# Optimization experiments

Measured on AMD Instinct MI355X. Metric: run time of the kernel, lower is better.

Reference implementation:

```python
import jax, jax.numpy as jnp
import numpy as np

B, N, C = 4, 2048, 320
H, D = 5, 64            # heads, dim_head
INNER = H * D           # 320


def setup_inputs() -> dict:
    key = jax.random.key(0)
    ks = jax.random.split(key, 7)
    x = jax.random.normal(ks[0], (B, N, C), dtype=jnp.float32)
    edge = jax.random.uniform(ks[1], (B, N, 1), dtype=jnp.float32)
    s = 1.0 / np.sqrt(C)
    Wq = jax.random.normal(ks[2], (C, INNER), dtype=jnp.float32) * s
    Wk = jax.random.normal(ks[3], (C, INNER), dtype=jnp.float32) * s
    Wv = jax.random.normal(ks[4], (C, INNER), dtype=jnp.float32) * s
    Wo = jax.random.normal(ks[5], (INNER, C), dtype=jnp.float32) * (1.0 / np.sqrt(INNER))
    bo = jnp.zeros((C,), dtype=jnp.float32)
    return {"x": x, "edge": edge, "Wq": Wq, "Wk": Wk, "Wv": Wv, "Wo": Wo, "bo": bo}


def _split_heads(t):
    # 'b n (h d) -> (b h) n d'  (batch-major, head-minor)
    b, n, _ = t.shape
    return t.reshape(b, n, H, D).transpose(0, 2, 1, 3).reshape(b * H, n, D)


def reference(x, edge, Wq, Wk, Wv, Wo, bo):
    scale = D ** -0.5
    q = _split_heads(x @ Wq).astype(jnp.float32)   # (B*H, N, D)
    k = _split_heads(x @ Wk).astype(jnp.float32)
    v = _split_heads(x @ Wv)

    sim = jnp.einsum('bid,bjd->bij', q, k) * scale  # (B*H, N, N)

    # torch: edge.repeat(h, 1, 1) -> batch-minor tiling; index i uses edge[i % B]
    edge_rep = jnp.tile(edge, (H, 1, 1))            # (H*B, N, 1)
    edge_matrix = edge_rep * edge_rep.transpose(0, 2, 1)  # outer product (H*B, N, N)

    sim = jax.nn.softmax(sim * edge_matrix, axis=-1)
    out = jnp.einsum('bij,bjd->bid', sim, v)        # (B*H, N, D)

    # '(b h) n d -> b n (h d)'
    out = out.reshape(B, H, N, D).transpose(0, 2, 1, 3).reshape(B, N, INNER)
    return out @ Wo + bo
```

## Files before the change

### kernel.cpp

```cpp
#include <hip/hip_runtime.h>
#include <hip/hip_bf16.h>
#include <math.h>


typedef short bf16x8 __attribute__((ext_vector_type(8)));
typedef float f32x4 __attribute__((ext_vector_type(4)));

static __device__ __forceinline__ ushort f2bf(float f) {
  union { float f; unsigned u; } v; v.f = f;
  unsigned r = (v.u + 0x7fffu + ((v.u >> 16) & 1u)) >> 16;
  return (ushort)r;
}
static __device__ __forceinline__ float fexp2(float x) {
#if __has_builtin(__builtin_amdgcn_exp2f)
  return __builtin_amdgcn_exp2f(x);
#else
  return exp2f(x);
#endif
}
static __device__ __forceinline__ f32x4 mfma32(bf16x8 a, bf16x8 b, f32x4 c) {
  return __builtin_amdgcn_mfma_f32_16x16x32_bf16(a, b, c, 0, 0, 0);
}

__global__ __launch_bounds__(256) void xcvt_kernel(
    const float* __restrict__ x, ushort* __restrict__ xb)
{
  const int t = threadIdx.x;
  const int mt2 = blockIdx.x;
  const int kc = blockIdx.y * 2 + (t >> 7);
  const int f = (t & 127) * 4;
  const int qq = f >> 7, mm = (f >> 3) & 15, e0 = f & 7;
  float4 v = *reinterpret_cast<const float4*>(
      x + (size_t)(mt2 * 16 + mm) * 320 + kc * 32 + qq * 8 + e0);
  ushort4 o = { f2bf(v.x), f2bf(v.y), f2bf(v.z), f2bf(v.w) };
  *reinterpret_cast<ushort4*>(xb + (size_t)(mt2 * 10 + kc) * 512 + f) = o;
}

__global__ __launch_bounds__(256) void wtrans_kernel(
    const float* __restrict__ Wq, const float* __restrict__ Wk,
    const float* __restrict__ Wv, const float* __restrict__ Wo,
    ushort* __restrict__ wt)
{
  const int z = blockIdx.z;
  const float* W = z == 0 ? Wq : z == 1 ? Wk : z == 2 ? Wv : Wo;
  const int nt2 = blockIdx.x, kc = blockIdx.y;
  const int f = threadIdx.x * 2;
  const int qq = f >> 7, nn = (f >> 3) & 15, e0 = f & 7;
  const int k = kc * 32 + qq * 8 + e0, n = nt2 * 16 + nn;
  float v0 = W[(size_t)k * 320 + n];
  float v1 = W[(size_t)(k + 1) * 320 + n];
  ushort2 o = { f2bf(v0), f2bf(v1) };
  *reinterpret_cast<ushort2*>(
      wt + (size_t)z * 102400 + (size_t)(nt2 * 10 + kc) * 512 + f) = o;
}

__global__ __launch_bounds__(256, 4) void qkv_gemm(
    const ushort* __restrict__ xb, const float* __restrict__ edge,
    const ushort* __restrict__ wt,
    ushort* __restrict__ qp, ushort* __restrict__ kS, ushort* __restrict__ vS)
{
  const int w = blockIdx.x;
  const int s = (w & 7) * 80 + (w >> 3);
  const int mt = s / 5, h = s % 5;
  const int wave = threadIdx.x >> 6, lane = threadIdx.x & 63;
  const int m16 = lane & 15, quad = lane >> 4;
  const int m0 = mt * 64 + wave * 16;
  const ushort* atile = xb + (size_t)(mt * 4 + wave) * 10 * 512 + lane * 8;
  const ushort* btile = wt + (size_t)(h * 4) * 10 * 512 + lane * 8;

  f32x4 acc[3][4];
#pragma unroll
  for (int z = 0; z < 3; ++z)
#pragma unroll
    for (int ns = 0; ns < 4; ++ns) acc[z][ns] = (f32x4){0.f, 0.f, 0.f, 0.f};

#pragma unroll
  for (int kc = 0; kc < 10; ++kc) {
    bf16x8 af = *reinterpret_cast<const bf16x8*>(atile + kc * 512);
#pragma unroll
    for (int z = 0; z < 3; ++z)
#pragma unroll
      for (int ns = 0; ns < 4; ++ns) {
        bf16x8 bf = *reinterpret_cast<const bf16x8*>(
            btile + (size_t)z * 102400 + (ns * 10 + kc) * 512);
        acc[z][ns] = mfma32(af, bf, acc[z][ns]);
      }
  }

  const float QSCALE = 0.18033688011112042f;
  const int mrow = m0 + quad * 4;
  const int b = mrow >> 11;
  const int n = mrow & 2047;
  const int bh = b * 5 + h;
  const float* eb = edge + (size_t)((b + h) & 3) * 2048;
  float e[4];
#pragma unroll
  for (int r = 0; r < 4; ++r) e[r] = eb[n + r];

  {
    ushort* dst = qp + ((size_t)bh * 2048 + n) * 64;
#pragma unroll
    for (int ns = 0; ns < 4; ++ns) {
      int d = ns * 16 + m16;
#pragma unroll
      for (int r = 0; r < 4; ++r)
        dst[(size_t)r * 64 + d] = f2bf(acc[0][ns][r] * e[r] * QSCALE);
    }
  }
  {
    const size_t base = (size_t)bh * 131072 + (size_t)((mt & 31) * 4 + wave) * 1024;
#pragma unroll
    for (int ns = 0; ns < 4; ++ns) {
      size_t a0 = base + (ns >> 1) * 512 +
                  (((ns & 1) * 2 + (m16 >> 3)) * 16 + quad * 4) * 8 + (m16 & 7);
#pragma unroll
      for (int r = 0; r < 4; ++r)
        kS[a0 + (size_t)r * 8] = f2bf(acc[1][ns][r] * e[r]);
    }
  }
  {
#pragma unroll
    for (int ns = 0; ns < 4; ++ns) {
      ushort4 o = { f2bf(acc[2][ns][0]), f2bf(acc[2][ns][1]),
                    f2bf(acc[2][ns][2]), f2bf(acc[2][ns][3]) };
      size_t addr = (size_t)bh * 131072 + (size_t)ns * 32768 +
                    (size_t)(mt & 31) * 1024 + (wave >> 1) * 512 +
                    (quad * 16 + m16) * 8 + (wave & 1) * 4;
      *reinterpret_cast<ushort4*>(vS + addr) = o;
    }
  }
}

__global__ __launch_bounds__(256, 2) void attn_kernel(
    const ushort* __restrict__ qp, const ushort* __restrict__ kS,
    const ushort* __restrict__ vS, ushort* __restrict__ ao)
{
  __shared__ f32x4 lo[3][16][64];
  __shared__ float lrs[4][4][16];
  const int w = blockIdx.x;
  const int s = (w & 7) * 80 + (w >> 3);
  const int bh = s >> 5, qt = s & 31;
  const int b = bh / 5, h = bh % 5;
  const int wave = threadIdx.x >> 6, lane = threadIdx.x & 63;
  const int m16 = lane & 15, quad = lane >> 4;
  const int q0 = qt * 64;

  bf16x8 qf[4][2];
#pragma unroll
  for (int qs = 0; qs < 4; ++qs) {
    const ushort* qrow = qp + ((size_t)bh * 2048 + q0 + qs * 16 + m16) * 64;
    qf[qs][0] = *reinterpret_cast<const bf16x8*>(qrow + quad * 8);
    qf[qs][1] = *reinterpret_cast<const bf16x8*>(qrow + 32 + quad * 8);
  }
  const ushort* kb_p = kS + (size_t)bh * 131072 + lane * 8;
  const ushort* vb_p = vS + (size_t)bh * 131072 + lane * 8;

  f32x4 oacc[4][4], rsacc[4];
#pragma unroll
  for (int qs = 0; qs < 4; ++qs) {
    rsacc[qs] = (f32x4){0.f, 0.f, 0.f, 0.f};
    for (int dt = 0; dt < 4; ++dt) oacc[qs][dt] = (f32x4){0.f, 0.f, 0.f, 0.f};
  }
  const bf16x8 ones8 = {(short)16256, (short)16256, (short)16256, (short)16256,
                        (short)16256, (short)16256, (short)16256, (short)16256};

  auto load_unit = [&](int u, bf16x8 kf[2][2], bf16x8 vf[4]) {
    const int jb = (u >> 1) * 4 + wave, kb = u & 1;
#pragma unroll
    for (int ss = 0; ss < 2; ++ss)
#pragma unroll
      for (int hf = 0; hf < 2; ++hf)
        kf[ss][hf] = *reinterpret_cast<const bf16x8*>(
            kb_p + (size_t)(jb * 4 + kb * 2 + ss) * 1024 + hf * 512);
#pragma unroll
    for (int dt = 0; dt < 4; ++dt)
      vf[dt] = *reinterpret_cast<const bf16x8*>(
          vb_p + (size_t)dt * 32768 + (size_t)jb * 1024 + kb * 512);
  };
  auto compute_unit = [&](bf16x8 kf[2][2], bf16x8 vf[4]) {
#pragma unroll
    for (int qs = 0; qs < 4; ++qs) {
      f32x4 st0 = (f32x4){0.f, 0.f, 0.f, 0.f};
      f32x4 st1 = (f32x4){0.f, 0.f, 0.f, 0.f};
      st0 = mfma32(kf[0][0], qf[qs][0], st0);
      st0 = mfma32(kf[0][1], qf[qs][1], st0);
      st1 = mfma32(kf[1][0], qf[qs][0], st1);
      st1 = mfma32(kf[1][1], qf[qs][1], st1);
      unsigned b0 = __float_as_uint(fexp2(st0[0]));
      unsigned b1 = __float_as_uint(fexp2(st0[1]));
      unsigned b2 = __float_as_uint(fexp2(st0[2]));
      unsigned b3 = __float_as_uint(fexp2(st0[3]));
      unsigned b4 = __float_as_uint(fexp2(st1[0]));
      unsigned b5 = __float_as_uint(fexp2(st1[1]));
      unsigned b6 = __float_as_uint(fexp2(st1[2]));
      unsigned b7 = __float_as_uint(fexp2(st1[3]));
      union { unsigned u[4]; bf16x8 v; } pk;
      pk.u[0] = __builtin_amdgcn_perm(b1, b0, 0x07060302u);
      pk.u[1] = __builtin_amdgcn_perm(b3, b2, 0x07060302u);
      pk.u[2] = __builtin_amdgcn_perm(b5, b4, 0x07060302u);
      pk.u[3] = __builtin_amdgcn_perm(b7, b6, 0x07060302u);
      rsacc[qs] = mfma32(ones8, pk.v, rsacc[qs]);
#pragma unroll
      for (int dt = 0; dt < 4; ++dt)
        oacc[qs][dt] = mfma32(vf[dt], pk.v, oacc[qs][dt]);
    }
  };

  bf16x8 kA[2][2], vA[4], kB[2][2], vB[4];
  load_unit(0, kA, vA);
#pragma unroll
  for (int u = 0; u < 16; u += 2) {
    load_unit(u + 1, kB, vB);
    compute_unit(kA, vA);
    if (u + 2 < 16) load_unit(u + 2, kA, vA);
    compute_unit(kB, vB);
  }

  if (wave > 0) {
#pragma unroll
    for (int qs = 0; qs < 4; ++qs)
#pragma unroll
      for (int dt = 0; dt < 4; ++dt)
        lo[wave - 1][qs * 4 + dt][lane] = oacc[qs][dt];
  }
  if (quad == 0) {
#pragma unroll
    for (int qs = 0; qs < 4; ++qs)
      lrs[wave][qs][m16] = rsacc[qs][0];
  }
  __syncthreads();
  if (wave == 0) {
#pragma unroll
    for (int qs = 0; qs < 4; ++qs) {
      float inv = 1.0f / (lrs[0][qs][m16] + lrs[1][qs][m16] +
                          lrs[2][qs][m16] + lrs[3][qs][m16]);
      const int mt2 = b * 128 + qt * 4 + qs;
#pragma unroll
      for (int dt = 0; dt < 4; ++dt) {
        f32x4 a = oacc[qs][dt];
        a += lo[0][qs * 4 + dt][lane];
        a += lo[1][qs * 4 + dt][lane];
        a += lo[2][qs * 4 + dt][lane];
        unsigned r0 = f2bf(a[0] * inv), r1 = f2bf(a[1] * inv);
        unsigned r2 = f2bf(a[2] * inv), r3 = f2bf(a[3] * inv);
        uint2 ww;
        ww.x = r0 | (r1 << 16);
        ww.y = r2 | (r3 << 16);
        size_t addr = (size_t)(mt2 * 10 + h * 2 + (dt >> 1)) * 512 +
                      ((((dt & 1) * 2 + (quad >> 1)) * 16 + m16)) * 8 +
                      (quad & 1) * 4;
        *reinterpret_cast<uint2*>(ao + addr) = ww;
      }
    }
  }
}

__global__ __launch_bounds__(256, 4) void oproj_gemm(
    const ushort* __restrict__ ao, const ushort* __restrict__ wt,
    const float* __restrict__ bo, float* __restrict__ out)
{
  const int w = blockIdx.x;
  const int s = (w & 7) * 80 + (w >> 3);
  const int mt = s / 5, ct = s % 5;
  const int wave = threadIdx.x >> 6, lane = threadIdx.x & 63;
  const int m16 = lane & 15, quad = lane >> 4;
  const int m0 = mt * 64 + wave * 16;
  const int n0 = ct * 64;
  const ushort* atile = ao + (size_t)(mt * 4 + wave) * 10 * 512 + lane * 8;
  const ushort* btile = wt + (size_t)3 * 102400 + (size_t)(ct * 4) * 10 * 512 + lane * 8;

  f32x4 acc[4];
#pragma unroll
  for (int ns = 0; ns < 4; ++ns) acc[ns] = (f32x4){0.f, 0.f, 0.f, 0.f};

#pragma unroll
  for (int kc = 0; kc < 10; ++kc) {
    bf16x8 af = *reinterpret_cast<const bf16x8*>(atile + kc * 512);
#pragma unroll
    for (int ns = 0; ns < 4; ++ns) {
      bf16x8 bf = *reinterpret_cast<const bf16x8*>(btile + (ns * 10 + kc) * 512);
      acc[ns] = mfma32(af, bf, acc[ns]);
    }
  }

  float bb[4];
#pragma unroll
  for (int ns = 0; ns < 4; ++ns) bb[ns] = bo[n0 + ns * 16 + m16];
  const int mrow = m0 + quad * 4;
#pragma unroll
  for (int ns = 0; ns < 4; ++ns)
#pragma unroll
    for (int r = 0; r < 4; ++r)
      out[(size_t)(mrow + r) * 320 + n0 + ns * 16 + m16] = acc[ns][r] + bb[ns];
}

extern "C" void kernel_launch(void* const* d_in, const int* in_sizes, int n_in,
                              void* d_out, int out_size, void* d_ws, size_t ws_size,
                              hipStream_t stream) {
  const float* x    = (const float*)d_in[0];
  const float* edge = (const float*)d_in[1];
  const float* Wq   = (const float*)d_in[2];
  const float* Wk   = (const float*)d_in[3];
  const float* Wv   = (const float*)d_in[4];
  const float* Wo   = (const float*)d_in[5];
  const float* bo   = (const float*)d_in[6];
  float* out = (float*)d_out;

  ushort* xb = (ushort*)d_ws;
  ushort* wt = xb + (size_t)8192 * 320;
  ushort* qp = wt + (size_t)4 * 320 * 320;
  ushort* kS = qp + (size_t)20 * 2048 * 64;
  ushort* vS = kS + (size_t)20 * 2048 * 64;
  ushort* ao = vS + (size_t)20 * 2048 * 64;

  xcvt_kernel<<<dim3(512, 5), 256, 0, stream>>>(x, xb);
  wtrans_kernel<<<dim3(20, 10, 4), 256, 0, stream>>>(Wq, Wk, Wv, Wo, wt);
  qkv_gemm<<<640, 256, 0, stream>>>(xb, edge, wt, qp, kS, vS);
  attn_kernel<<<640, 256, 0, stream>>>(qp, kS, vS, ao);
  oproj_gemm<<<640, 256, 0, stream>>>(ao, wt, bo, out);
}
```

Before: 153.2 us.

## Retile QKV and output GEMMs to 64x64 per wave, halve attention query tile

The QKV GEMM now gives each wave a 64x64 output tile for a single projection (q, k or v) instead of a 16-row strip across all three. This raises operand reuse per load and changes the grid to 480 blocks. The output projection gets the same 64x64 per-wave tiling with 128-thread blocks. The attention kernel processes 32 query rows per block instead of 64, doubling the grid to 1280 blocks for more parallelism, and adds sched_barriers to pin the load/compute interleave. Smaller attention tiles reread K/V more often, and larger GEMM tiles mean fewer blocks.

```diff
diff --git a/kernel.cpp b/kernel.cpp
--- a/kernel.cpp
+++ b/kernel.cpp
@@ -60,73 +60,90 @@
     ushort* __restrict__ qp, ushort* __restrict__ kS, ushort* __restrict__ vS)
 {
   const int w = blockIdx.x;
-  const int s = (w & 7) * 80 + (w >> 3);
-  const int mt = s / 5, h = s % 5;
+  const int s = (w & 7) * 60 + (w >> 3);
+  const int mg = s / 15, zh = s % 15;
+  const int z = zh / 5, h = zh % 5;
   const int wave = threadIdx.x >> 6, lane = threadIdx.x & 63;
   const int m16 = lane & 15, quad = lane >> 4;
-  const int m0 = mt * 64 + wave * 16;
-  const ushort* atile = xb + (size_t)(mt * 4 + wave) * 10 * 512 + lane * 8;
-  const ushort* btile = wt + (size_t)(h * 4) * 10 * 512 + lane * 8;
-
-  f32x4 acc[3][4];
-#pragma unroll
-  for (int z = 0; z < 3; ++z)
-#pragma unroll
-    for (int ns = 0; ns < 4; ++ns) acc[z][ns] = (f32x4){0.f, 0.f, 0.f, 0.f};
+  const int m0 = mg * 256 + wave * 64;
+  const int row16 = m0 >> 4;
+  const ushort* atile = xb + (size_t)row16 * 5120 + lane * 8;
+  const ushort* btile = wt + (size_t)z * 102400 + (size_t)(h * 4) * 5120 + lane * 8;
+
+  f32x4 acc[4][4];
+#pragma unroll
+  for (int i = 0; i < 4; ++i)
+#pragma unroll
+    for (int ns = 0; ns < 4; ++ns) acc[i][ns] = (f32x4){0.f, 0.f, 0.f, 0.f};
 
 #pragma unroll
   for (int kc = 0; kc < 10; ++kc) {
-    bf16x8 af = *reinterpret_cast<const bf16x8*>(atile + kc * 512);
-#pragma unroll
-    for (int z = 0; z < 3; ++z)
-#pragma unroll
-      for (int ns = 0; ns < 4; ++ns) {
-        bf16x8 bf = *reinterpret_cast<const bf16x8*>(
-            btile + (size_t)z * 102400 + (ns * 10 + kc) * 512);
-        acc[z][ns] = mfma32(af, bf, acc[z][ns]);
-      }
+    bf16x8 af[4], bf[4];
+#pragma unroll
+    for (int i = 0; i < 4; ++i)
+      af[i] = *reinterpret_cast<const bf16x8*>(atile + (i * 10 + kc) * 512);
+#pragma unroll
+    for (int ns = 0; ns < 4; ++ns)
+      bf[ns] = *reinterpret_cast<const bf16x8*>(btile + (ns * 10 + kc) * 512);
+#pragma unroll
+    for (int i = 0; i < 4; ++i)
+#pragma unroll
+      for (int ns = 0; ns < 4; ++ns)
+        acc[i][ns] = mfma32(af[i], bf[ns], acc[i][ns]);
   }
 
   const float QSCALE = 0.18033688011112042f;
-  const int mrow = m0 + quad * 4;
-  const int b = mrow >> 11;
-  const int n = mrow & 2047;
+  const int b = m0 >> 11;
   const int bh = b * 5 + h;
   const float* eb = edge + (size_t)((b + h) & 3) * 2048;
-  float e[4];
-#pragma unroll
-  for (int r = 0; r < 4; ++r) e[r] = eb[n + r];
-
-  {
-    ushort* dst = qp + ((size_t)bh * 2048 + n) * 64;
-#pragma unroll
-    for (int ns = 0; ns < 4; ++ns) {
-      int d = ns * 16 + m16;
-#pragma unroll
-      for (int r = 0; r < 4; ++r)
-        dst[(size_t)r * 64 + d] = f2bf(acc[0][ns][r] * e[r] * QSCALE);
-    }
-  }
-  {
-    const size_t base = (size_t)bh * 131072 + (size_t)((mt & 31) * 4 + wave) * 1024;
-#pragma unroll
-    for (int ns = 0; ns < 4; ++ns) {
-      size_t a0 = base + (ns >> 1) * 512 +
-                  (((ns & 1) * 2 + (m16 >> 3)) * 16 + quad * 4) * 8 + (m16 & 7);
-#pragma unroll
-      for (int r = 0; r < 4; ++r)
-        kS[a0 + (size_t)r * 8] = f2bf(acc[1][ns][r] * e[r]);
-    }
-  }
-  {
-#pragma unroll
-    for (int ns = 0; ns < 4; ++ns) {
-      ushort4 o = { f2bf(acc[2][ns][0]), f2bf(acc[2][ns][1]),
-                    f2bf(acc[2][ns][2]), f2bf(acc[2][ns][3]) };
-      size_t addr = (size_t)bh * 131072 + (size_t)ns * 32768 +
-                    (size_t)(mt & 31) * 1024 + (wave >> 1) * 512 +
-                    (quad * 16 + m16) * 8 + (wave & 1) * 4;
-      *reinterpret_cast<ushort4*>(vS + addr) = o;
+  const int nwb = m0 & 2047;
+
+  if (z == 0) {
+#pragma unroll
+    for (int i = 0; i < 4; ++i) {
+      const int nb = nwb + i * 16 + quad * 4;
+      float e[4];
+#pragma unroll
+      for (int r = 0; r < 4; ++r) e[r] = eb[nb + r] * QSCALE;
+      ushort* dst = qp + ((size_t)bh * 2048 + nb) * 64;
+#pragma unroll
+      for (int ns = 0; ns < 4; ++ns)
+#pragma unroll
+        for (int r = 0; r < 4; ++r)
+          dst[(size_t)r * 64 + ns * 16 + m16] = f2bf(acc[i][ns][r] * e[r]);
+    }
+  } else if (z == 1) {
+#pragma unroll
+    for (int i = 0; i < 4; ++i) {
+      const int nb = nwb + i * 16 + quad * 4;
+      float e[4];
+#pragma unroll
+      for (int r = 0; r < 4; ++r) e[r] = eb[nb + r];
+      const int j16 = ((m0 >> 4) + i) & 127;
+      const size_t base = (size_t)bh * 131072 + (size_t)j16 * 1024;
+#pragma unroll
+      for (int ns = 0; ns < 4; ++ns) {
+        size_t a0 = base + (ns >> 1) * 512 +
+                    (((ns & 1) * 2 + (m16 >> 3)) * 16 + quad * 4) * 8 + (m16 & 7);
+#pragma unroll
+        for (int r = 0; r < 4; ++r)
+          kS[a0 + (size_t)r * 8] = f2bf(acc[i][ns][r] * e[r]);
+      }
+    }
+  } else {
+    const int jb = nwb >> 6;
+#pragma unroll
+    for (int i = 0; i < 4; ++i) {
+      const int kb = i >> 1, e4 = (i & 1) * 4;
+#pragma unroll
+      for (int ns = 0; ns < 4; ++ns) {
+        ushort4 o = { f2bf(acc[i][ns][0]), f2bf(acc[i][ns][1]),
+                      f2bf(acc[i][ns][2]), f2bf(acc[i][ns][3]) };
+        size_t addr = (size_t)bh * 131072 + (size_t)ns * 32768 +
+                      (size_t)jb * 1024 + kb * 512 +
+                      (quad * 16 + m16) * 8 + e4;
+        *reinterpret_cast<ushort4*>(vS + addr) = o;
+      }
     }
   }
 }
@@ -135,19 +152,19 @@
     const ushort* __restrict__ qp, const ushort* __restrict__ kS,
     const ushort* __restrict__ vS, ushort* __restrict__ ao)
 {
-  __shared__ f32x4 lo[3][16][64];
-  __shared__ float lrs[4][4][16];
+  __shared__ f32x4 lo[3][8][64];
+  __shared__ float lrs[4][2][16];
   const int w = blockIdx.x;
-  const int s = (w & 7) * 80 + (w >> 3);
-  const int bh = s >> 5, qt = s & 31;
+  const int s = (w & 7) * 160 + (w >> 3);
+  const int bh = s >> 6, qt = s & 63;
   const int b = bh / 5, h = bh % 5;
   const int wave = threadIdx.x >> 6, lane = threadIdx.x & 63;
   const int m16 = lane & 15, quad = lane >> 4;
-  const int q0 = qt * 64;
-
-  bf16x8 qf[4][2];
-#pragma unroll
-  for (int qs = 0; qs < 4; ++qs) {
+  const int q0 = qt * 32;
+
+  bf16x8 qf[2][2];
+#pragma unroll
+  for (int qs = 0; qs < 2; ++qs) {
     const ushort* qrow = qp + ((size_t)bh * 2048 + q0 + qs * 16 + m16) * 64;
     qf[qs][0] = *reinterpret_cast<const bf16x8*>(qrow + quad * 8);
     qf[qs][1] = *reinterpret_cast<const bf16x8*>(qrow + 32 + quad * 8);
@@ -155,9 +172,9 @@
   const ushort* kb_p = kS + (size_t)bh * 131072 + lane * 8;
   const ushort* vb_p = vS + (size_t)bh * 131072 + lane * 8;
 
-  f32x4 oacc[4][4], rsacc[4];
-#pragma unroll
-  for (int qs = 0; qs < 4; ++qs) {
+  f32x4 oacc[2][4], rsacc[2];
+#pragma unroll
+  for (int qs = 0; qs < 2; ++qs) {
     rsacc[qs] = (f32x4){0.f, 0.f, 0.f, 0.f};
     for (int dt = 0; dt < 4; ++dt) oacc[qs][dt] = (f32x4){0.f, 0.f, 0.f, 0.f};
   }
@@ -179,7 +196,7 @@
   };
   auto compute_unit = [&](bf16x8 kf[2][2], bf16x8 vf[4]) {
 #pragma unroll
-    for (int qs = 0; qs < 4; ++qs) {
+    for (int qs = 0; qs < 2; ++qs) {
       f32x4 st0 = (f32x4){0.f, 0.f, 0.f, 0.f};
       f32x4 st1 = (f32x4){0.f, 0.f, 0.f, 0.f};
       st0 = mfma32(kf[0][0], qf[qs][0], st0);
@@ -208,33 +225,36 @@
 
   bf16x8 kA[2][2], vA[4], kB[2][2], vB[4];
   load_unit(0, kA, vA);
+  __builtin_amdgcn_sched_barrier(0);
 #pragma unroll
   for (int u = 0; u < 16; u += 2) {
     load_unit(u + 1, kB, vB);
+    __builtin_amdgcn_sched_barrier(0);
     compute_unit(kA, vA);
     if (u + 2 < 16) load_unit(u + 2, kA, vA);
+    __builtin_amdgcn_sched_barrier(0);
     compute_unit(kB, vB);
+    __builtin_amdgcn_sched_barrier(0);
   }
 
   if (wave > 0) {
 #pragma unroll
-    for (int qs = 0; qs < 4; ++qs)
+    for (int qs = 0; qs < 2; ++qs)
 #pragma unroll
       for (int dt = 0; dt < 4; ++dt)
         lo[wave - 1][qs * 4 + dt][lane] = oacc[qs][dt];
   }
   if (quad == 0) {
-#pragma unroll
-    for (int qs = 0; qs < 4; ++qs)
-      lrs[wave][qs][m16] = rsacc[qs][0];
+    lrs[wave][0][m16] = rsacc[0][0];
+    lrs[wave][1][m16] = rsacc[1][0];
   }
   __syncthreads();
   if (wave == 0) {
 #pragma unroll
-    for (int qs = 0; qs < 4; ++qs) {
+    for (int qs = 0; qs < 2; ++qs) {
       float inv = 1.0f / (lrs[0][qs][m16] + lrs[1][qs][m16] +
                           lrs[2][qs][m16] + lrs[3][qs][m16]);
-      const int mt2 = b * 128 + qt * 4 + qs;
+      const int mt2 = b * 128 + qt * 2 + qs;
 #pragma unroll
       for (int dt = 0; dt < 4; ++dt) {
         f32x4 a = oacc[qs][dt];
@@ -255,43 +275,54 @@
   }
 }
 
-__global__ __launch_bounds__(256, 4) void oproj_gemm(
+__global__ __launch_bounds__(128, 4) void oproj_gemm(
     const ushort* __restrict__ ao, const ushort* __restrict__ wt,
     const float* __restrict__ bo, float* __restrict__ out)
 {
   const int w = blockIdx.x;
-  const int s = (w & 7) * 80 + (w >> 3);
-  const int mt = s / 5, ct = s % 5;
+  const int s = (w & 7) * 40 + (w >> 3);
+  const int mg = s / 5, ct = s % 5;
   const int wave = threadIdx.x >> 6, lane = threadIdx.x & 63;
   const int m16 = lane & 15, quad = lane >> 4;
-  const int m0 = mt * 64 + wave * 16;
+  const int m0 = mg * 128 + wave * 64;
   const int n0 = ct * 64;
-  const ushort* atile = ao + (size_t)(mt * 4 + wave) * 10 * 512 + lane * 8;
-  const ushort* btile = wt + (size_t)3 * 102400 + (size_t)(ct * 4) * 10 * 512 + lane * 8;
-
-  f32x4 acc[4];
-#pragma unroll
-  for (int ns = 0; ns < 4; ++ns) acc[ns] = (f32x4){0.f, 0.f, 0.f, 0.f};
+  const ushort* atile = ao + (size_t)(m0 >> 4) * 5120 + lane * 8;
+  const ushort* btile = wt + (size_t)3 * 102400 + (size_t)(ct * 4) * 5120 + lane * 8;
+
+  f32x4 acc[4][4];
+#pragma unroll
+  for (int i = 0; i < 4; ++i)
+#pragma unroll
+    for (int ns = 0; ns < 4; ++ns) acc[i][ns] = (f32x4){0.f, 0.f, 0.f, 0.f};
 
 #pragma unroll
   for (int kc = 0; kc < 10; ++kc) {
-    bf16x8 af = *reinterpret_cast<const bf16x8*>(atile + kc * 512);
-#pragma unroll
-    for (int ns = 0; ns < 4; ++ns) {
-      bf16x8 bf = *reinterpret_cast<const bf16x8*>(btile + (ns * 10 + kc) * 512);
-      acc[ns] = mfma32(af, bf, acc[ns]);
-    }
+    bf16x8 af[4], bf[4];
+#pragma unroll
+    for (int i = 0; i < 4; ++i)
+      af[i] = *reinterpret_cast<const bf16x8*>(atile + (i * 10 + kc) * 512);
+#pragma unroll
+    for (int ns = 0; ns < 4; ++ns)
+      bf[ns] = *reinterpret_cast<const bf16x8*>(btile + (ns * 10 + kc) * 512);
+#pragma unroll
+    for (int i = 0; i < 4; ++i)
+#pragma unroll
+      for (int ns = 0; ns < 4; ++ns)
+        acc[i][ns] = mfma32(af[i], bf[ns], acc[i][ns]);
   }
 
   float bb[4];
 #pragma unroll
   for (int ns = 0; ns < 4; ++ns) bb[ns] = bo[n0 + ns * 16 + m16];
-  const int mrow = m0 + quad * 4;
-#pragma unroll
-  for (int ns = 0; ns < 4; ++ns)
-#pragma unroll
-    for (int r = 0; r < 4; ++r)
-      out[(size_t)(mrow + r) * 320 + n0 + ns * 16 + m16] = acc[ns][r] + bb[ns];
+#pragma unroll
+  for (int i = 0; i < 4; ++i) {
+    const int mrow = m0 + i * 16 + quad * 4;
+#pragma unroll
+    for (int ns = 0; ns < 4; ++ns)
+#pragma unroll
+      for (int r = 0; r < 4; ++r)
+        out[(size_t)(mrow + r) * 320 + n0 + ns * 16 + m16] = acc[i][ns][r] + bb[ns];
+  }
 }
 
 extern "C" void kernel_launch(void* const* d_in, const int* in_sizes, int n_in,
@@ -315,7 +346,7 @@
 
   xcvt_kernel<<<dim3(512, 5), 256, 0, stream>>>(x, xb);
   wtrans_kernel<<<dim3(20, 10, 4), 256, 0, stream>>>(Wq, Wk, Wv, Wo, wt);
-  qkv_gemm<<<640, 256, 0, stream>>>(xb, edge, wt, qp, kS, vS);
-  attn_kernel<<<640, 256, 0, stream>>>(qp, kS, vS, ao);
-  oproj_gemm<<<640, 256, 0, stream>>>(ao, wt, bo, out);
-}
+  qkv_gemm<<<480, 256, 0, stream>>>(xb, edge, wt, qp, kS, vS);
+  attn_kernel<<<1280, 256, 0, stream>>>(qp, kS, vS, ao);
+  oproj_gemm<<<320, 128, 0, stream>>>(ao, wt, bo, out);
+}
```

After: 134.0 us. 1.14x faster.
